# Kernel optimization log

Hardware: AMD Instinct MI355X
Metric: run time of the kernel (lower is better)

Reference implementation:

```python
import jax, jax.numpy as jnp
import numpy as np


def setup_inputs() -> dict:
    key = jax.random.key(0)
    k_in, k_w, k_b = jax.random.split(key, 3)
    B, S, H, HEADS = 16, 4096, 768, 8
    inputs = jax.random.normal(k_in, (B, S, H), dtype=jnp.float32)
    # xavier_uniform for Linear(H -> HEADS): limit = sqrt(6/(fan_in+fan_out))
    limit = float(np.sqrt(6.0 / (H + HEADS)))
    W = jax.random.uniform(k_w, (HEADS, H), dtype=jnp.float32, minval=-limit, maxval=limit)
    b = jnp.zeros((HEADS,), dtype=jnp.float32)  # nn.Linear default bias init left as zeros-equivalent scale; use uniform per torch default
    bound = float(1.0 / np.sqrt(H))
    b = jax.random.uniform(k_b, (HEADS,), dtype=jnp.float32, minval=-bound, maxval=bound)
    return {"inputs": inputs, "W": W, "b": b}


def reference(inputs, W, b):
    # atten = Linear(inputs) -> [B, S, heads]; transpose -> [B, heads, S]
    atten = jnp.einsum("bsh,eh->bes", inputs, W) + b[None, :, None]  # [B, heads, S]
    atten_sm = jax.nn.softmax(atten, axis=-1)                        # softmax over seq
    out = jnp.einsum("bes,bsh->beh", atten_sm, inputs)               # [B, heads, H]
    return (out, atten)
```

## Files before the change

### kernel.cpp

```cpp
#include <hip/hip_runtime.h>
#include <hip/hip_bf16.h>
#include <math.h>

constexpr int Bn = 16;
constexpr int Sn = 4096;
constexpr int Hn = 768;
constexpr int En = 8;
constexpr int OUT_N = Bn * En * Hn;
constexpr int NBLK  = 512;
constexpr int NSC   = 32;

__global__ __launch_bounds__(256, 2) void k_fused(
    const float* __restrict__ x, const float* __restrict__ W,
    const float* __restrict__ bias, float* __restrict__ att,
    float* __restrict__ part, float* __restrict__ sumexpG) {
  const int lane = threadIdx.x & 63;
  const int w    = threadIdx.x >> 6;
  const int wid  = blockIdx.x * 4 + w;
  const int b    = wid >> 7;
  const int wl   = wid & 127;

  float4 wf[8][3];
#pragma unroll
  for (int e = 0; e < 8; ++e)
#pragma unroll
    for (int j = 0; j < 3; ++j)
      wf[e][j] = *(const float4*)(W + e * 768 + (lane << 2) + (j << 8));
  const float bv = bias[lane & 7];

  float4 acc[8][3];
#pragma unroll
  for (int e = 0; e < 8; ++e)
#pragma unroll
    for (int j = 0; j < 3; ++j) acc[e][j] = make_float4(0.f, 0.f, 0.f, 0.f);
  float sume = 0.0f;

  int r = b * Sn + wl;
  const float4* rp = (const float4*)(x + (size_t)r * Hn);
  float4 c0 = rp[lane], c1 = rp[lane + 64], c2 = rp[lane + 128];

  for (int t = 0; t < 32; ++t) {
    const bool more = (t + 1 < 32);
    float4 n0, n1, n2;
    if (more) {
      const float4* np_ = (const float4*)(x + (size_t)(r + 128) * Hn);
      n0 = np_[lane]; n1 = np_[lane + 64]; n2 = np_[lane + 128];
    }

    float a8[8];
#pragma unroll
    for (int e = 0; e < 8; ++e) {
      float a = c0.x * wf[e][0].x;
      a = fmaf(c0.y, wf[e][0].y, a);
      a = fmaf(c0.z, wf[e][0].z, a);
      a = fmaf(c0.w, wf[e][0].w, a);
      a = fmaf(c1.x, wf[e][1].x, a);
      a = fmaf(c1.y, wf[e][1].y, a);
      a = fmaf(c1.z, wf[e][1].z, a);
      a = fmaf(c1.w, wf[e][1].w, a);
      a = fmaf(c2.x, wf[e][2].x, a);
      a = fmaf(c2.y, wf[e][2].y, a);
      a = fmaf(c2.z, wf[e][2].z, a);
      a = fmaf(c2.w, wf[e][2].w, a);
      a8[e] = a;
    }

    float v4[4];
#pragma unroll
    for (int k = 0; k < 4; ++k) {
      const float pa = a8[2 * k], pb = a8[2 * k + 1];
      const bool hi = (lane & 1);
      const float send = hi ? pa : pb;
      const float keep = hi ? pb : pa;
      v4[k] = keep + __shfl_xor(send, 1, 64);
    }
    float v2[2];
#pragma unroll
    for (int k = 0; k < 2; ++k) {
      const float pa = v4[2 * k], pb = v4[2 * k + 1];
      const bool hi = (lane & 2);
      const float send = hi ? pa : pb;
      const float keep = hi ? pb : pa;
      v2[k] = keep + __shfl_xor(send, 2, 64);
    }
    float u;
    {
      const float pa = v2[0], pb = v2[1];
      const bool hi = (lane & 4);
      const float send = hi ? pa : pb;
      const float keep = hi ? pb : pa;
      u = keep + __shfl_xor(send, 4, 64);
    }
    u += __shfl_xor(u, 8, 64);
    u += __shfl_xor(u, 16, 64);
    u += __shfl_xor(u, 32, 64);

    const float logit = u + bv;
    if (lane < 8)
      att[(size_t)((b << 3) + lane) * Sn + (r & 4095)] = logit;

    const float texp = __expf(logit);
    sume += texp;

#pragma unroll
    for (int e = 0; e < 8; ++e) {
      const float we = __shfl(texp, e, 64);
      acc[e][0].x = fmaf(we, c0.x, acc[e][0].x);
      acc[e][0].y = fmaf(we, c0.y, acc[e][0].y);
      acc[e][0].z = fmaf(we, c0.z, acc[e][0].z);
      acc[e][0].w = fmaf(we, c0.w, acc[e][0].w);
      acc[e][1].x = fmaf(we, c1.x, acc[e][1].x);
      acc[e][1].y = fmaf(we, c1.y, acc[e][1].y);
      acc[e][1].z = fmaf(we, c1.z, acc[e][1].z);
      acc[e][1].w = fmaf(we, c1.w, acc[e][1].w);
      acc[e][2].x = fmaf(we, c2.x, acc[e][2].x);
      acc[e][2].y = fmaf(we, c2.y, acc[e][2].y);
      acc[e][2].z = fmaf(we, c2.z, acc[e][2].z);
      acc[e][2].w = fmaf(we, c2.w, acc[e][2].w);
    }

    if (!more) break;
    r += 128;
    c0 = n0; c1 = n1; c2 = n2;
  }

  __shared__ float4 lacc[3 * 24 * 64];
  __shared__ float  lsum[32];
  if (w > 0) {
    float4* dst = &lacc[(w - 1) * 24 * 64];
#pragma unroll
    for (int e = 0; e < 8; ++e)
#pragma unroll
      for (int j = 0; j < 3; ++j)
        dst[(e * 3 + j) * 64 + lane] = acc[e][j];
  }
  if (lane < 8) lsum[w * 8 + lane] = sume;
  __syncthreads();

  if (w == 0) {
#pragma unroll
    for (int g = 0; g < 3; ++g) {
      const float4* src = &lacc[g * 24 * 64];
#pragma unroll
      for (int e = 0; e < 8; ++e)
#pragma unroll
        for (int j = 0; j < 3; ++j) {
          const float4 v = src[(e * 3 + j) * 64 + lane];
          acc[e][j].x += v.x; acc[e][j].y += v.y;
          acc[e][j].z += v.z; acc[e][j].w += v.w;
        }
    }
    float4* po = (float4*)(part + (size_t)blockIdx.x * (En * Hn));
#pragma unroll
    for (int e = 0; e < 8; ++e)
#pragma unroll
      for (int j = 0; j < 3; ++j)
        po[e * 192 + j * 64 + lane] = acc[e][j];
    if (lane < 8)
      sumexpG[blockIdx.x * 8 + lane] =
          lsum[lane] + lsum[8 + lane] + lsum[16 + lane] + lsum[24 + lane];
  }
}

__global__ __launch_bounds__(256) void k_final(const float* __restrict__ part,
                                               const float* __restrict__ sumexpG,
                                               float* __restrict__ out) {
  __shared__ float Zs[128];
  const int t = threadIdx.x;
  if (t < 128) {
    const int b = t >> 3, e = t & 7;
    float z = 0.0f;
    for (int c = 0; c < NSC; ++c) z += sumexpG[((b * NSC + c) << 3) + e];
    Zs[t] = 1.0f / z;
  }
  __syncthreads();

  const int o4 = blockIdx.x * 256 + t;
  const int b  = o4 / 1536;
  const int r4 = o4 - b * 1536;
  const int e  = r4 / 192;
  const float4* p4 = (const float4*)part + (size_t)(b * NSC) * 1536 + r4;
  float4 a = make_float4(0.f, 0.f, 0.f, 0.f);
  for (int c = 0; c < NSC; ++c) {
    const float4 v = p4[(size_t)c * 1536];
    a.x += v.x; a.y += v.y; a.z += v.z; a.w += v.w;
  }
  const float inv = Zs[(b << 3) + e];
  a.x *= inv; a.y *= inv; a.z *= inv; a.w *= inv;
  ((float4*)out)[o4] = a;
}

extern "C" void kernel_launch(void* const* d_in, const int* in_sizes, int n_in,
                              void* d_out, int out_size, void* d_ws, size_t ws_size,
                              hipStream_t stream) {
  const float* x    = (const float*)d_in[0];
  const float* W    = (const float*)d_in[1];
  const float* bias = (const float*)d_in[2];
  float* out = (float*)d_out;
  float* att = out + OUT_N;
  float* part    = (float*)d_ws;
  float* sumexpG = part + NBLK * En * Hn;

  k_fused<<<NBLK, 256, 0, stream>>>(x, W, bias, att, part, sumexpG);
  k_final<<<OUT_N / 4 / 256, 256, 0, stream>>>(part, sumexpG, out);
}
```

Measured before the change: 285.8 us.

## Split heads across waves and share rows via double-buffered LDS

Each wave now owns two of the eight heads instead of all eight. The four waves of a block cooperatively stage four input rows per round into a double-buffered shared-memory tile, and every wave reads all four rows from LDS. This cuts per-thread registers (accumulators and weights drop from 24 float4 to 6 each), allowing 4 blocks per CU and twice as many blocks, and it removes the end-of-block LDS reduction. The cost is LDS traffic, a __syncthreads per round, twice as many partials for the final kernel to sum, and a full 64-lane shuffle reduction per head pair.

```diff
diff --git a/kernel.cpp b/kernel.cpp
--- a/kernel.cpp
+++ b/kernel.cpp
@@ -1,165 +1,153 @@
 #include <hip/hip_runtime.h>
-#include <hip/hip_bf16.h>
 #include <math.h>
 
 constexpr int Bn = 16;
 constexpr int Sn = 4096;
 constexpr int Hn = 768;
 constexpr int En = 8;
-constexpr int OUT_N = Bn * En * Hn;
-constexpr int NBLK  = 512;
-constexpr int NSC   = 32;
+constexpr int OUT_N  = Bn * En * Hn;
+constexpr int NBLK   = 1024;
+constexpr int NSC    = 64;
+constexpr int ROUNDS = 16;
 
-__global__ __launch_bounds__(256, 2) void k_fused(
+__device__ __forceinline__ float dot12(const float4 c0, const float4 c1,
+                                       const float4 c2, const float4 w0,
+                                       const float4 w1, const float4 w2) {
+  float a = c0.x * w0.x;
+  a = fmaf(c0.y, w0.y, a); a = fmaf(c0.z, w0.z, a); a = fmaf(c0.w, w0.w, a);
+  a = fmaf(c1.x, w1.x, a); a = fmaf(c1.y, w1.y, a); a = fmaf(c1.z, w1.z, a);
+  a = fmaf(c1.w, w1.w, a);
+  a = fmaf(c2.x, w2.x, a); a = fmaf(c2.y, w2.y, a); a = fmaf(c2.z, w2.z, a);
+  a = fmaf(c2.w, w2.w, a);
+  return a;
+}
+
+__device__ __forceinline__ void fma4(float4& a, const float s, const float4 c) {
+  a.x = fmaf(s, c.x, a.x); a.y = fmaf(s, c.y, a.y);
+  a.z = fmaf(s, c.z, a.z); a.w = fmaf(s, c.w, a.w);
+}
+
+__global__ __launch_bounds__(256, 4) void k_fused(
     const float* __restrict__ x, const float* __restrict__ W,
     const float* __restrict__ bias, float* __restrict__ att,
     float* __restrict__ part, float* __restrict__ sumexpG) {
+  __shared__ float buf[2][4][Hn];
   const int lane = threadIdx.x & 63;
   const int w    = threadIdx.x >> 6;
-  const int wid  = blockIdx.x * 4 + w;
-  const int b    = wid >> 7;
-  const int wl   = wid & 127;
+  const int blk  = blockIdx.x;
+  const int b    = blk >> 6;
+  const int ib   = blk & 63;
 
-  float4 wf[8][3];
+  float4 wf[2][3];
 #pragma unroll
-  for (int e = 0; e < 8; ++e)
+  for (int p = 0; p < 2; ++p)
 #pragma unroll
-    for (int j = 0; j < 3; ++j)
-      wf[e][j] = *(const float4*)(W + e * 768 + (lane << 2) + (j << 8));
-  const float bv = bias[lane & 7];
+    for (int c = 0; c < 3; ++c)
+      wf[p][c] = *(const float4*)(W + (2 * w + p) * Hn + (c << 8) + (lane << 2));
+  const float bvp = bias[2 * w + (lane & 1)];
 
-  float4 acc[8][3];
+  float4 acc[2][3];
 #pragma unroll
-  for (int e = 0; e < 8; ++e)
+  for (int p = 0; p < 2; ++p)
 #pragma unroll
-    for (int j = 0; j < 3; ++j) acc[e][j] = make_float4(0.f, 0.f, 0.f, 0.f);
+    for (int c = 0; c < 3; ++c) acc[p][c] = make_float4(0.f, 0.f, 0.f, 0.f);
   float sume = 0.0f;
 
-  int r = b * Sn + wl;
-  const float4* rp = (const float4*)(x + (size_t)r * Hn);
-  float4 c0 = rp[lane], c1 = rp[lane + 64], c2 = rp[lane + 128];
+  const float* xb = x + (size_t)b * Sn * Hn;
+  float* attw = att + (size_t)(b * En + 2 * w) * Sn;
 
-  for (int t = 0; t < 32; ++t) {
-    const bool more = (t + 1 < 32);
-    float4 n0, n1, n2;
+  float4 st0, st1, st2;
+  {
+    const float* rp = xb + (size_t)((w << 6) + ib) * Hn;
+    st0 = *(const float4*)(rp + (lane << 2));
+    st1 = *(const float4*)(rp + 256 + (lane << 2));
+    st2 = *(const float4*)(rp + 512 + (lane << 2));
+  }
+  {
+    float* d = &buf[0][w][0];
+    *(float4*)(d + (lane << 2)) = st0;
+    *(float4*)(d + 256 + (lane << 2)) = st1;
+    *(float4*)(d + 512 + (lane << 2)) = st2;
+  }
+  __syncthreads();
+
+  for (int t = 0; t < ROUNDS; ++t) {
+    const int cur = t & 1;
+    const bool more = (t + 1 < ROUNDS);
     if (more) {
-      const float4* np_ = (const float4*)(x + (size_t)(r + 128) * Hn);
-      n0 = np_[lane]; n1 = np_[lane + 64]; n2 = np_[lane + 128];
+      const float* rp = xb + (size_t)(((4 * (t + 1) + w) << 6) + ib) * Hn;
+      st0 = *(const float4*)(rp + (lane << 2));
+      st1 = *(const float4*)(rp + 256 + (lane << 2));
+      st2 = *(const float4*)(rp + 512 + (lane << 2));
     }
 
-    float a8[8];
+    float4 ra0, ra1, ra2, rb0, rb1, rb2;
+    {
+      const float* s0 = &buf[cur][0][0];
+      ra0 = *(const float4*)(s0 + (lane << 2));
+      ra1 = *(const float4*)(s0 + 256 + (lane << 2));
+      ra2 = *(const float4*)(s0 + 512 + (lane << 2));
+    }
 #pragma unroll
-    for (int e = 0; e < 8; ++e) {
-      float a = c0.x * wf[e][0].x;
-      a = fmaf(c0.y, wf[e][0].y, a);
-      a = fmaf(c0.z, wf[e][0].z, a);
-      a = fmaf(c0.w, wf[e][0].w, a);
-      a = fmaf(c1.x, wf[e][1].x, a);
-      a = fmaf(c1.y, wf[e][1].y, a);
-      a = fmaf(c1.z, wf[e][1].z, a);
-      a = fmaf(c1.w, wf[e][1].w, a);
-      a = fmaf(c2.x, wf[e][2].x, a);
-      a = fmaf(c2.y, wf[e][2].y, a);
-      a = fmaf(c2.z, wf[e][2].z, a);
-      a = fmaf(c2.w, wf[e][2].w, a);
-      a8[e] = a;
+    for (int rr = 0; rr < 4; ++rr) {
+      const float4 c0 = (rr & 1) ? rb0 : ra0;
+      const float4 c1 = (rr & 1) ? rb1 : ra1;
+      const float4 c2 = (rr & 1) ? rb2 : ra2;
+      if (rr < 3) {
+        const float* sn = &buf[cur][rr + 1][0];
+        if (rr & 1) {
+          ra0 = *(const float4*)(sn + (lane << 2));
+          ra1 = *(const float4*)(sn + 256 + (lane << 2));
+          ra2 = *(const float4*)(sn + 512 + (lane << 2));
+        } else {
+          rb0 = *(const float4*)(sn + (lane << 2));
+          rb1 = *(const float4*)(sn + 256 + (lane << 2));
+          rb2 = *(const float4*)(sn + 512 + (lane << 2));
+        }
+      }
+
+      const float a0 = dot12(c0, c1, c2, wf[0][0], wf[0][1], wf[0][2]);
+      const float a1 = dot12(c0, c1, c2, wf[1][0], wf[1][1], wf[1][2]);
+
+      const bool hi = (lane & 1);
+      const float send = hi ? a0 : a1;
+      const float keep = hi ? a1 : a0;
+      float v = keep + __shfl_xor(send, 1, 64);
+      v += __shfl_xor(v, 2, 64);
+      v += __shfl_xor(v, 4, 64);
+      v += __shfl_xor(v, 8, 64);
+      v += __shfl_xor(v, 16, 64);
+      v += __shfl_xor(v, 32, 64);
+
+      const float logit = v + bvp;
+      const int s = (((t << 2) + rr) << 6) + ib;
+      if (lane < 2) attw[(size_t)lane * Sn + s] = logit;
+
+      const float texp = __expf(logit);
+      sume += texp;
+      const float we0 = __shfl(texp, 0, 64);
+      const float we1 = __shfl(texp, 1, 64);
+      fma4(acc[0][0], we0, c0); fma4(acc[0][1], we0, c1); fma4(acc[0][2], we0, c2);
+      fma4(acc[1][0], we1, c0); fma4(acc[1][1], we1, c1); fma4(acc[1][2], we1, c2);
     }
 
-    float v4[4];
-#pragma unroll
-    for (int k = 0; k < 4; ++k) {
-      const float pa = a8[2 * k], pb = a8[2 * k + 1];
-      const bool hi = (lane & 1);
-      const float send = hi ? pa : pb;
-      const float keep = hi ? pb : pa;
-      v4[k] = keep + __shfl_xor(send, 1, 64);
+    if (more) {
+      float* d = &buf[cur ^ 1][w][0];
+      *(float4*)(d + (lane << 2)) = st0;
+      *(float4*)(d + 256 + (lane << 2)) = st1;
+      *(float4*)(d + 512 + (lane << 2)) = st2;
     }
-    float v2[2];
-#pragma unroll
-    for (int k = 0; k < 2; ++k) {
-      const float pa = v4[2 * k], pb = v4[2 * k + 1];
-      const bool hi = (lane & 2);
-      const float send = hi ? pa : pb;
-      const float keep = hi ? pb : pa;
-      v2[k] = keep + __shfl_xor(send, 2, 64);
-    }
-    float u;
-    {
-      const float pa = v2[0], pb = v2[1];
-      const bool hi = (lane & 4);
-      const float send = hi ? pa : pb;
-      const float keep = hi ? pb : pa;
-      u = keep + __shfl_xor(send, 4, 64);
-    }
-    u += __shfl_xor(u, 8, 64);
-    u += __shfl_xor(u, 16, 64);
-    u += __shfl_xor(u, 32, 64);
-
-    const float logit = u + bv;
-    if (lane < 8)
-      att[(size_t)((b << 3) + lane) * Sn + (r & 4095)] = logit;
-
-    const float texp = __expf(logit);
-    sume += texp;
-
-#pragma unroll
-    for (int e = 0; e < 8; ++e) {
-      const float we = __shfl(texp, e, 64);
-      acc[e][0].x = fmaf(we, c0.x, acc[e][0].x);
-      acc[e][0].y = fmaf(we, c0.y, acc[e][0].y);
-      acc[e][0].z = fmaf(we, c0.z, acc[e][0].z);
-      acc[e][0].w = fmaf(we, c0.w, acc[e][0].w);
-      acc[e][1].x = fmaf(we, c1.x, acc[e][1].x);
-      acc[e][1].y = fmaf(we, c1.y, acc[e][1].y);
-      acc[e][1].z = fmaf(we, c1.z, acc[e][1].z);
-      acc[e][1].w = fmaf(we, c1.w, acc[e][1].w);
-      acc[e][2].x = fmaf(we, c2.x, acc[e][2].x);
-      acc[e][2].y = fmaf(we, c2.y, acc[e][2].y);
-      acc[e][2].z = fmaf(we, c2.z, acc[e][2].z);
-      acc[e][2].w = fmaf(we, c2.w, acc[e][2].w);
-    }
-
-    if (!more) break;
-    r += 128;
-    c0 = n0; c1 = n1; c2 = n2;
+    __syncthreads();
   }
 
-  __shared__ float4 lacc[3 * 24 * 64];
-  __shared__ float  lsum[32];
-  if (w > 0) {
-    float4* dst = &lacc[(w - 1) * 24 * 64];
+  float* po = part + (size_t)blk * (En * Hn) + (size_t)(2 * w) * Hn;
 #pragma unroll
-    for (int e = 0; e < 8; ++e)
-#pragma unroll
-      for (int j = 0; j < 3; ++j)
-        dst[(e * 3 + j) * 64 + lane] = acc[e][j];
+  for (int p = 0; p < 2; ++p) {
+    *(float4*)(po + p * Hn + (lane << 2))       = acc[p][0];
+    *(float4*)(po + p * Hn + 256 + (lane << 2)) = acc[p][1];
+    *(float4*)(po + p * Hn + 512 + (lane << 2)) = acc[p][2];
   }
-  if (lane < 8) lsum[w * 8 + lane] = sume;
-  __syncthreads();
-
-  if (w == 0) {
-#pragma unroll
-    for (int g = 0; g < 3; ++g) {
-      const float4* src = &lacc[g * 24 * 64];
-#pragma unroll
-      for (int e = 0; e < 8; ++e)
-#pragma unroll
-        for (int j = 0; j < 3; ++j) {
-          const float4 v = src[(e * 3 + j) * 64 + lane];
-          acc[e][j].x += v.x; acc[e][j].y += v.y;
-          acc[e][j].z += v.z; acc[e][j].w += v.w;
-        }
-    }
-    float4* po = (float4*)(part + (size_t)blockIdx.x * (En * Hn));
-#pragma unroll
-    for (int e = 0; e < 8; ++e)
-#pragma unroll
-      for (int j = 0; j < 3; ++j)
-        po[e * 192 + j * 64 + lane] = acc[e][j];
-    if (lane < 8)
-      sumexpG[blockIdx.x * 8 + lane] =
-          lsum[lane] + lsum[8 + lane] + lsum[16 + lane] + lsum[24 + lane];
-  }
+  if (lane < 2) sumexpG[(blk << 3) + 2 * w + lane] = sume;
 }
 
 __global__ __launch_bounds__(256) void k_final(const float* __restrict__ part,
```

Result: slower. 309.1 us (+8.2%).

## Stream input rows through a per-wave LDS ring buffer via global_load_lds

Applied to the files above, without the earlier changes.

Replaces the register double-buffer of the next row with a 5-slot per-wavefront LDS FIFO filled by direct global-to-LDS loads, keeping four rows in flight. The waits use explicit vmcnt counts. The intent is deeper memory-level parallelism to hide HBM latency on this bandwidth-bound pass over the input, and lower register pressure. The cross-wave accumulator reduction now reuses the same LDS in two halves to fit the budget, which adds extra barriers. The hand-tuned vmcnt values depend on the att global stores also being counted, which is fragile.

```diff
diff --git a/kernel.cpp b/kernel.cpp
--- a/kernel.cpp
+++ b/kernel.cpp
@@ -1,5 +1,4 @@
 #include <hip/hip_runtime.h>
-#include <hip/hip_bf16.h>
 #include <math.h>
 
 constexpr int Bn = 16;
@@ -9,11 +8,18 @@
 constexpr int OUT_N = Bn * En * Hn;
 constexpr int NBLK  = 512;
 constexpr int NSC   = 32;
+constexpr int SLOTS = 5;
+constexpr int WFSZ  = SLOTS * Hn;
+constexpr int LSUM  = 4 * WFSZ;
+
+typedef const __attribute__((address_space(1))) void gvoid;
+typedef __attribute__((address_space(3))) void svoid;
 
 __global__ __launch_bounds__(256, 2) void k_fused(
     const float* __restrict__ x, const float* __restrict__ W,
     const float* __restrict__ bias, float* __restrict__ att,
     float* __restrict__ part, float* __restrict__ sumexpG) {
+  __shared__ float sh[4 * WFSZ + 32];
   const int lane = threadIdx.x & 63;
   const int w    = threadIdx.x >> 6;
   const int wid  = blockIdx.x * 4 + w;
@@ -35,17 +41,26 @@
     for (int j = 0; j < 3; ++j) acc[e][j] = make_float4(0.f, 0.f, 0.f, 0.f);
   float sume = 0.0f;
 
-  int r = b * Sn + wl;
-  const float4* rp = (const float4*)(x + (size_t)r * Hn);
-  float4 c0 = rp[lane], c1 = rp[lane + 64], c2 = rp[lane + 128];
-
+  float* fifo = sh + w * WFSZ;
+  const float* xr = x + (size_t)(b * Sn + wl) * Hn;
+
+#pragma unroll
+  for (int k = 0; k < 4; ++k) {
+    const float* rp = xr + (size_t)(k * 128) * Hn;
+    float* dst = fifo + k * Hn;
+#pragma unroll
+    for (int c = 0; c < 3; ++c)
+      __builtin_amdgcn_global_load_lds((gvoid*)(rp + (c << 8) + (lane << 2)),
+                                       (svoid*)(dst + (c << 8)), 16, 0, 0);
+  }
+
+  int sp = 0, pf = 4;
   for (int t = 0; t < 32; ++t) {
-    const bool more = (t + 1 < 32);
-    float4 n0, n1, n2;
-    if (more) {
-      const float4* np_ = (const float4*)(x + (size_t)(r + 128) * Hn);
-      n0 = np_[lane]; n1 = np_[lane + 64]; n2 = np_[lane + 128];
-    }
+    if (t < 30) asm volatile("s_waitcnt vmcnt(9)" ::: "memory");
+    else        asm volatile("s_waitcnt vmcnt(0)" ::: "memory");
+
+    const float4* s4 = (const float4*)(fifo + sp * Hn);
+    const float4 c0 = s4[lane], c1 = s4[lane + 64], c2 = s4[lane + 128];
 
     float a8[8];
 #pragma unroll
@@ -96,8 +111,8 @@
     u += __shfl_xor(u, 32, 64);
 
     const float logit = u + bv;
-    if (lane < 8)
-      att[(size_t)((b << 3) + lane) * Sn + (r & 4095)] = logit;
+    const int s = wl + (t << 7);
+    if (lane < 8) att[(size_t)((b << 3) + lane) * Sn + s] = logit;
 
     const float texp = __expf(logit);
     sume += texp;
@@ -119,37 +134,47 @@
       acc[e][2].w = fmaf(we, c2.w, acc[e][2].w);
     }
 
-    if (!more) break;
-    r += 128;
-    c0 = n0; c1 = n1; c2 = n2;
-  }
-
-  __shared__ float4 lacc[3 * 24 * 64];
-  __shared__ float  lsum[32];
-  if (w > 0) {
-    float4* dst = &lacc[(w - 1) * 24 * 64];
-#pragma unroll
-    for (int e = 0; e < 8; ++e)
-#pragma unroll
-      for (int j = 0; j < 3; ++j)
-        dst[(e * 3 + j) * 64 + lane] = acc[e][j];
-  }
-  if (lane < 8) lsum[w * 8 + lane] = sume;
-  __syncthreads();
-
+    if (t < 28) {
+      const float* rp = xr + (size_t)((t + 4) * 128) * Hn;
+      float* dst = fifo + pf * Hn;
+#pragma unroll
+      for (int c = 0; c < 3; ++c)
+        __builtin_amdgcn_global_load_lds((gvoid*)(rp + (c << 8) + (lane << 2)),
+                                         (svoid*)(dst + (c << 8)), 16, 0, 0);
+    }
+    sp = (sp + 1 == SLOTS) ? 0 : sp + 1;
+    pf = (pf + 1 == SLOTS) ? 0 : pf + 1;
+  }
+
+  if (lane < 8) sh[LSUM + w * 8 + lane] = sume;
+#pragma unroll
+  for (int half = 0; half < 2; ++half) {
+    __syncthreads();
+    if (w > 0) {
+      float4* dst = (float4*)sh + (size_t)(w - 1) * 768;
+#pragma unroll
+      for (int e = 0; e < 4; ++e)
+#pragma unroll
+        for (int j = 0; j < 3; ++j)
+          dst[(e * 3 + j) * 64 + lane] = acc[half * 4 + e][j];
+    }
+    __syncthreads();
+    if (w == 0) {
+#pragma unroll
+      for (int g = 0; g < 3; ++g) {
+        const float4* src = (const float4*)sh + (size_t)g * 768;
+#pragma unroll
+        for (int e = 0; e < 4; ++e)
+#pragma unroll
+          for (int j = 0; j < 3; ++j) {
+            const float4 v = src[(e * 3 + j) * 64 + lane];
+            float4& a = acc[half * 4 + e][j];
+            a.x += v.x; a.y += v.y; a.z += v.z; a.w += v.w;
+          }
+      }
+    }
+  }
   if (w == 0) {
-#pragma unroll
-    for (int g = 0; g < 3; ++g) {
-      const float4* src = &lacc[g * 24 * 64];
-#pragma unroll
-      for (int e = 0; e < 8; ++e)
-#pragma unroll
-        for (int j = 0; j < 3; ++j) {
-          const float4 v = src[(e * 3 + j) * 64 + lane];
-          acc[e][j].x += v.x; acc[e][j].y += v.y;
-          acc[e][j].z += v.z; acc[e][j].w += v.w;
-        }
-    }
     float4* po = (float4*)(part + (size_t)blockIdx.x * (En * Hn));
 #pragma unroll
     for (int e = 0; e < 8; ++e)
@@ -157,8 +182,8 @@
       for (int j = 0; j < 3; ++j)
         po[e * 192 + j * 64 + lane] = acc[e][j];
     if (lane < 8)
-      sumexpG[blockIdx.x * 8 + lane] =
-          lsum[lane] + lsum[8 + lane] + lsum[16 + lane] + lsum[24 + lane];
+      sumexpG[blockIdx.x * 8 + lane] = sh[LSUM + lane] + sh[LSUM + 8 + lane] +
+                                       sh[LSUM + 16 + lane] + sh[LSUM + 24 + lane];
   }
 }
 
```

Result: no change. 287.8 us (+0.7%).
